# Performance work log

Hardware: AMD Instinct MI355X
Metric: run time of the kernel (lower is better)

The kernel has to match this reference:

```python
import jax, jax.numpy as jnp
import numpy as np

D, J, K, H = 4, 256, 512, 512  # d, num_output, num_input, num_hidden
B = 1024


def setup_inputs() -> dict:
    key = jax.random.key(0)
    ks = jax.random.split(key, 8)
    x = jax.random.normal(ks[0], (B, K), dtype=jnp.float32)
    # self.w = ((1-0.1)*U + 0.1) / num_input, shape [d, num_output, num_input]
    w = ((0.9 * jax.random.uniform(ks[1], (D, J, K), dtype=jnp.float32) + 0.1) / K)
    # Stacked per-output-MLP params (nn.Linear default init scale 1/sqrt(fan_in))
    s0 = 1.0 / np.sqrt(K)
    s1 = 1.0 / np.sqrt(H)
    W0 = jax.random.uniform(ks[2], (J, H, K), dtype=jnp.float32, minval=-s0, maxval=s0)
    b0 = jax.random.uniform(ks[3], (J, H), dtype=jnp.float32, minval=-s0, maxval=s0)
    W1 = jax.random.uniform(ks[4], (J, H), dtype=jnp.float32, minval=-s1, maxval=s1)  # [J,1,H] squeezed
    b1 = jax.random.uniform(ks[5], (J,), dtype=jnp.float32, minval=-s1, maxval=s1)
    logvar = jnp.ones((D,), dtype=jnp.float32) * -4.0
    return {"x": x, "i": 0, "w": w, "W0": W0, "b0": b0, "W1": W1, "b1": b1, "logvar": logvar}


def reference(x, i, w, W0, b0, W1, b1, logvar):
    # For each output j: mu[:, j] = lin1_j(LeakyReLU(lin0_j(w[i, j] * x)))
    # Fused as a single grouped GEMM over j: fold the mask w[i] into the contraction.
    wi = w[i]                                   # [J, K]
    h = jnp.einsum('jhk,jk,bk->bjh', W0, wi, x) + b0[None, :, :]   # [B, J, H]
    h = jax.nn.leaky_relu(h, negative_slope=0.01)
    mu = jnp.einsum('bjh,jh->bj', h, W1) + b1[None, :]             # [B, J]
    return (mu, logvar)
```

## Files before the change

kernel.cpp:

```cpp
#include <hip/hip_runtime.h>

#define J_ 256
#define K_ 512
#define H_ 512
#define B_ 1024
#define BK 64

typedef float f32x4 __attribute__((ext_vector_type(4)));
typedef unsigned int u32x4 __attribute__((ext_vector_type(4)));
typedef unsigned short u16x4 __attribute__((ext_vector_type(4)));
typedef unsigned short u16x8 __attribute__((ext_vector_type(8)));
typedef __bf16 bf16x8 __attribute__((ext_vector_type(8)));

__device__ __forceinline__ unsigned short f2bf(float f) {
    unsigned int u = __float_as_uint(f);
    u += 0x7fffu + ((u >> 16) & 1u);
    return (unsigned short)(u >> 16);
}

__global__ __launch_bounds__(256) void prep_kernel(
    const float* __restrict__ x, const float* __restrict__ b1,
    const float* __restrict__ logvar, unsigned short* __restrict__ xbf,
    float* __restrict__ out) {
    int t = blockIdx.x * 256 + threadIdx.x;
    {
        f32x4 v = *(const f32x4*)(x + (size_t)t * 4);
        u16x4 o;
        o[0] = f2bf(v[0]); o[1] = f2bf(v[1]); o[2] = f2bf(v[2]); o[3] = f2bf(v[3]);
        *(u16x4*)(xbf + (size_t)t * 4) = o;
    }
    if (t < (B_ * J_) / 4) {
        int b = t >> 6;
        int j4 = (t & 63) << 2;
        f32x4 bb = *(const f32x4*)(b1 + j4);
        *(f32x4*)(out + ((size_t)b << 8) + j4) = bb;
    }
    if (t < 4) out[B_ * J_ + t] = logvar[t];
}

__global__ __launch_bounds__(256, 2) void enc_kernel(
    const unsigned short* __restrict__ xbf,
    const float* __restrict__ W0,
    const float* __restrict__ wmask,
    const int* __restrict__ ip,
    const float* __restrict__ b0,
    const float* __restrict__ W1,
    float* __restrict__ out) {
    __shared__ unsigned char ldsA[128 * 128];
    __shared__ unsigned char ldsB[128 * 128];

    int p = blockIdx.x;
    int xcd = p & 7;
    int q = p >> 3;
    int j = (xcd << 5) + (q >> 5);
    int inner = q & 31;
    int m0 = (inner >> 2) << 7;
    int h0 = (inner & 3) << 7;

    int i = ip[0];
    const float* w0j = W0 + (size_t)j * (H_ * K_);
    const float* wij = wmask + ((size_t)i * J_ + j) * K_;

    int tid = threadIdx.x;
    int lane = tid & 63;
    int wv = tid >> 6;
    int wm = wv >> 1, wn = wv & 1;
    int lr = lane & 15, lg = lane >> 4;

    int srow0 = tid >> 3;
    int c = tid & 7;

    f32x4 acc[4][4] = {};

    for (int ks = 0; ks < K_ / BK; ++ks) {
        int k0 = ks * BK;
        #pragma unroll
        for (int it = 0; it < 4; ++it) {
            int r = srow0 + it * 32;
            u32x4 v = *(const u32x4*)(xbf + (size_t)(m0 + r) * K_ + k0 + c * 8);
            *(u32x4*)(ldsA + r * 128 + ((c * 16) ^ ((r & 7) << 4))) = v;
        }
        f32x4 s0 = *(const f32x4*)(wij + k0 + c * 8);
        f32x4 s1 = *(const f32x4*)(wij + k0 + c * 8 + 4);
        #pragma unroll
        for (int it = 0; it < 4; ++it) {
            int hr = srow0 + it * 32;
            const float* src = w0j + (size_t)(h0 + hr) * K_ + k0 + c * 8;
            f32x4 a0 = *(const f32x4*)(src);
            f32x4 a1 = *(const f32x4*)(src + 4);
            a0 *= s0; a1 *= s1;
            u16x8 bv;
            #pragma unroll
            for (int e = 0; e < 4; ++e) { bv[e] = f2bf(a0[e]); bv[e + 4] = f2bf(a1[e]); }
            *(u16x8*)(ldsB + hr * 128 + ((c * 16) ^ ((hr & 7) << 4))) = bv;
        }
        __syncthreads();
        #pragma unroll
        for (int kf = 0; kf < 2; ++kf) {
            bf16x8 af[4], bfr[4];
            #pragma unroll
            for (int mf = 0; mf < 4; ++mf) {
                int r = (wm << 6) + (mf << 4) + lr;
                af[mf] = *(const bf16x8*)(ldsA + r * 128 +
                          (((kf << 6) + (lg << 4)) ^ ((r & 7) << 4)));
            }
            #pragma unroll
            for (int nf = 0; nf < 4; ++nf) {
                int hrw = (wn << 6) + (nf << 4) + lr;
                bfr[nf] = *(const bf16x8*)(ldsB + hrw * 128 +
                          (((kf << 6) + (lg << 4)) ^ ((hrw & 7) << 4)));
            }
            #pragma unroll
            for (int mf = 0; mf < 4; ++mf)
                #pragma unroll
                for (int nf = 0; nf < 4; ++nf)
                    acc[mf][nf] = __builtin_amdgcn_mfma_f32_16x16x32_bf16(
                        af[mf], bfr[nf], acc[mf][nf], 0, 0, 0);
        }
        __syncthreads();
    }

    float b0v[4], w1v[4];
    #pragma unroll
    for (int nf = 0; nf < 4; ++nf) {
        int h = h0 + (wn << 6) + (nf << 4) + lr;
        b0v[nf] = b0[(size_t)j * H_ + h];
        w1v[nf] = W1[(size_t)j * H_ + h];
    }
    #pragma unroll
    for (int mf = 0; mf < 4; ++mf) {
        #pragma unroll
        for (int rg = 0; rg < 4; ++rg) {
            float ps = 0.f;
            #pragma unroll
            for (int nf = 0; nf < 4; ++nf) {
                float hv = acc[mf][nf][rg] + b0v[nf];
                hv = hv > 0.f ? hv : 0.01f * hv;
                ps += hv * w1v[nf];
            }
            ps += __shfl_xor(ps, 1);
            ps += __shfl_xor(ps, 2);
            ps += __shfl_xor(ps, 4);
            ps += __shfl_xor(ps, 8);
            if (lr == 0) {
                int row = m0 + (wm << 6) + (mf << 4) + (lg << 2) + rg;
                atomicAdd(out + (size_t)row * J_ + j, ps);
            }
        }
    }
}

extern "C" void kernel_launch(void* const* d_in, const int* in_sizes, int n_in,
                              void* d_out, int out_size, void* d_ws, size_t ws_size,
                              hipStream_t stream) {
    const float* x      = (const float*)d_in[0];
    const int*   ip     = (const int*)d_in[1];
    const float* wmask  = (const float*)d_in[2];
    const float* W0     = (const float*)d_in[3];
    const float* b0     = (const float*)d_in[4];
    const float* W1     = (const float*)d_in[5];
    const float* b1     = (const float*)d_in[6];
    const float* logvar = (const float*)d_in[7];
    float* out = (float*)d_out;
    unsigned short* xbf = (unsigned short*)d_ws;

    prep_kernel<<<512, 256, 0, stream>>>(x, b1, logvar, xbf, out);
    enc_kernel<<<8192, 256, 0, stream>>>(xbf, W0, wmask, ip, b0, W1, out);
}
```

Measured before the change: 582.9 us.

## Pre-convert masked W0 to bf16 and stream tiles via global_load_lds

Measured after the change: 582.4 us. About the same (-0.1%).

```diff
diff --git a/kernel.cpp b/kernel.cpp
--- a/kernel.cpp
+++ b/kernel.cpp
@@ -16,6 +16,12 @@
     unsigned int u = __float_as_uint(f);
     u += 0x7fffu + ((u >> 16) & 1u);
     return (unsigned short)(u >> 16);
+}
+
+__device__ __forceinline__ void gload_lds16(const void* g, void* l) {
+    __builtin_amdgcn_global_load_lds(
+        (const __attribute__((address_space(1))) unsigned int*)g,
+        (__attribute__((address_space(3))) unsigned int*)l, 16, 0, 0);
 }
 
 __global__ __launch_bounds__(256) void prep_kernel(
@@ -38,7 +44,122 @@
     if (t < 4) out[B_ * J_ + t] = logvar[t];
 }
 
-__global__ __launch_bounds__(256, 2) void enc_kernel(
+__global__ __launch_bounds__(256) void wprep_kernel(
+    const float* __restrict__ W0, const float* __restrict__ wmask,
+    const int* __restrict__ ip, unsigned short* __restrict__ w0p) {
+    size_t t = (size_t)blockIdx.x * 256 + threadIdx.x;
+    size_t e = t * 8;
+    int j = (int)(e >> 18);
+    int k = (int)(e & (K_ - 1));
+    const float* wi = wmask + ((size_t)ip[0] * J_ + j) * K_ + k;
+    f32x4 s0 = *(const f32x4*)wi;
+    f32x4 s1 = *(const f32x4*)(wi + 4);
+    f32x4 a0 = *(const f32x4*)(W0 + e);
+    f32x4 a1 = *(const f32x4*)(W0 + e + 4);
+    a0 *= s0; a1 *= s1;
+    u16x8 o;
+    #pragma unroll
+    for (int q = 0; q < 4; ++q) { o[q] = f2bf(a0[q]); o[q + 4] = f2bf(a1[q]); }
+    *(u16x8*)(w0p + e) = o;
+}
+
+__global__ __launch_bounds__(256, 3) void enc_kernel(
+    const unsigned short* __restrict__ xbf,
+    const unsigned short* __restrict__ w0p,
+    const float* __restrict__ b0,
+    const float* __restrict__ W1,
+    float* __restrict__ out) {
+    __shared__ unsigned char ldsA[128 * 128];
+    __shared__ unsigned char ldsB[128 * 128];
+
+    int p = blockIdx.x;
+    int xcd = p & 7;
+    int q = p >> 3;
+    int j = (xcd << 5) + (q >> 5);
+    int inner = q & 31;
+    int m0 = (inner >> 2) << 7;
+    int h0 = (inner & 3) << 7;
+
+    int tid = threadIdx.x;
+    int lane = tid & 63;
+    int wv = tid >> 6;
+    int wm = wv >> 1, wn = wv & 1;
+    int lr = lane & 15, lg = lane >> 4;
+    int lrow = lane >> 3;
+    int lch = lane & 7;
+    int sch = ((lch ^ lrow) << 3);
+
+    const unsigned short* aBase = xbf + (size_t)(m0 + wv * 32 + lrow) * K_ + sch;
+    const unsigned short* bBase = w0p + ((size_t)j * H_ + h0 + wv * 32 + lrow) * K_ + sch;
+    unsigned char* laBase = ldsA + wv * 4096;
+    unsigned char* lbBase = ldsB + wv * 4096;
+
+    f32x4 acc[4][4] = {};
+
+    for (int ks = 0; ks < K_ / BK; ++ks) {
+        int k0 = ks * BK;
+        #pragma unroll
+        for (int ii = 0; ii < 4; ++ii) {
+            gload_lds16(aBase + (size_t)ii * 8 * K_ + k0, laBase + ii * 1024);
+            gload_lds16(bBase + (size_t)ii * 8 * K_ + k0, lbBase + ii * 1024);
+        }
+        __syncthreads();
+        #pragma unroll
+        for (int kf = 0; kf < 2; ++kf) {
+            bf16x8 af[4], bfr[4];
+            #pragma unroll
+            for (int mf = 0; mf < 4; ++mf) {
+                int r = (wm << 6) + (mf << 4) + lr;
+                af[mf] = *(const bf16x8*)(ldsA + r * 128 +
+                          (((kf << 6) + (lg << 4)) ^ ((r & 7) << 4)));
+            }
+            #pragma unroll
+            for (int nf = 0; nf < 4; ++nf) {
+                int hrw = (wn << 6) + (nf << 4) + lr;
+                bfr[nf] = *(const bf16x8*)(ldsB + hrw * 128 +
+                          (((kf << 6) + (lg << 4)) ^ ((hrw & 7) << 4)));
+            }
+            #pragma unroll
+            for (int mf = 0; mf < 4; ++mf)
+                #pragma unroll
+                for (int nf = 0; nf < 4; ++nf)
+                    acc[mf][nf] = __builtin_amdgcn_mfma_f32_16x16x32_bf16(
+                        af[mf], bfr[nf], acc[mf][nf], 0, 0, 0);
+        }
+        __syncthreads();
+    }
+
+    float b0v[4], w1v[4];
+    #pragma unroll
+    for (int nf = 0; nf < 4; ++nf) {
+        int h = h0 + (wn << 6) + (nf << 4) + lr;
+        b0v[nf] = b0[(size_t)j * H_ + h];
+        w1v[nf] = W1[(size_t)j * H_ + h];
+    }
+    #pragma unroll
+    for (int mf = 0; mf < 4; ++mf) {
+        #pragma unroll
+        for (int rg = 0; rg < 4; ++rg) {
+            float ps = 0.f;
+            #pragma unroll
+            for (int nf = 0; nf < 4; ++nf) {
+                float hv = acc[mf][nf][rg] + b0v[nf];
+                hv = hv > 0.f ? hv : 0.01f * hv;
+                ps += hv * w1v[nf];
+            }
+            ps += __shfl_xor(ps, 1);
+            ps += __shfl_xor(ps, 2);
+            ps += __shfl_xor(ps, 4);
+            ps += __shfl_xor(ps, 8);
+            if (lr == 0) {
+                int row = m0 + (wm << 6) + (mf << 4) + (lg << 2) + rg;
+                atomicAdd(out + (size_t)row * J_ + j, ps);
+            }
+        }
+    }
+}
+
+__global__ __launch_bounds__(256, 2) void enc_kernel_fb(
     const unsigned short* __restrict__ xbf,
     const float* __restrict__ W0,
     const float* __restrict__ wmask,
@@ -66,7 +187,6 @@
     int wv = tid >> 6;
     int wm = wv >> 1, wn = wv & 1;
     int lr = lane & 15, lg = lane >> 4;
-
     int srow0 = tid >> 3;
     int c = tid & 7;
 
@@ -163,7 +283,16 @@
     const float* logvar = (const float*)d_in[7];
     float* out = (float*)d_out;
     unsigned short* xbf = (unsigned short*)d_ws;
+    const size_t xbf_elems = (size_t)B_ * K_;
+    const size_t w0p_bytes = (size_t)J_ * H_ * K_ * 2;
+    const size_t need = xbf_elems * 2 + w0p_bytes;
 
     prep_kernel<<<512, 256, 0, stream>>>(x, b1, logvar, xbf, out);
-    enc_kernel<<<8192, 256, 0, stream>>>(xbf, W0, wmask, ip, b0, W1, out);
-}
+    if (ws_size >= need) {
+        unsigned short* w0p = xbf + xbf_elems;
+        wprep_kernel<<<32768, 256, 0, stream>>>(W0, wmask, ip, w0p);
+        enc_kernel<<<8192, 256, 0, stream>>>(xbf, w0p, b0, W1, out);
+    } else {
+        enc_kernel_fb<<<8192, 256, 0, stream>>>(xbf, W0, wmask, ip, b0, W1, out);
+    }
+}
```

## Keep masked W0 slice resident in LDS and loop over all batch tiles

Applied to the files above, without the earlier changes.

Result: no change. 573.1 us (-1.7%).

```diff
diff --git a/kernel.cpp b/kernel.cpp
--- a/kernel.cpp
+++ b/kernel.cpp
@@ -7,7 +7,6 @@
 #define BK 64
 
 typedef float f32x4 __attribute__((ext_vector_type(4)));
-typedef unsigned int u32x4 __attribute__((ext_vector_type(4)));
 typedef unsigned short u16x4 __attribute__((ext_vector_type(4)));
 typedef unsigned short u16x8 __attribute__((ext_vector_type(8)));
 typedef __bf16 bf16x8 __attribute__((ext_vector_type(8)));
@@ -16,6 +15,12 @@
     unsigned int u = __float_as_uint(f);
     u += 0x7fffu + ((u >> 16) & 1u);
     return (unsigned short)(u >> 16);
+}
+
+__device__ __forceinline__ void gload_lds16(const void* g, void* l) {
+    __builtin_amdgcn_global_load_lds(
+        (const __attribute__((address_space(1))) unsigned int*)g,
+        (__attribute__((address_space(3))) unsigned int*)l, 16, 0, 0);
 }
 
 __global__ __launch_bounds__(256) void prep_kernel(
@@ -46,105 +51,111 @@
     const float* __restrict__ b0,
     const float* __restrict__ W1,
     float* __restrict__ out) {
-    __shared__ unsigned char ldsA[128 * 128];
-    __shared__ unsigned char ldsB[128 * 128];
+    __shared__ unsigned char ldsB[64 * 1024];
+    __shared__ unsigned char ldsX[128 * 128];
 
     int p = blockIdx.x;
-    int xcd = p & 7;
-    int q = p >> 3;
-    int j = (xcd << 5) + (q >> 5);
-    int inner = q & 31;
-    int m0 = (inner >> 2) << 7;
-    int h0 = (inner & 3) << 7;
-
-    int i = ip[0];
-    const float* w0j = W0 + (size_t)j * (H_ * K_);
-    const float* wij = wmask + ((size_t)i * J_ + j) * K_;
+    int j = p >> 3;
+    int hb = p & 7;
+    int h0 = hb << 6;
 
     int tid = threadIdx.x;
     int lane = tid & 63;
     int wv = tid >> 6;
-    int wm = wv >> 1, wn = wv & 1;
     int lr = lane & 15, lg = lane >> 4;
 
-    int srow0 = tid >> 3;
-    int c = tid & 7;
+    {
+        const float* w0p = W0 + ((size_t)j * H_ + h0) * K_;
+        const float* wij = wmask + ((size_t)ip[0] * J_ + j) * K_;
+        int row = (wv << 4) + lr;
+        int cb = lg;
+        const float* src = w0p + (size_t)row * K_;
+        unsigned int swb = ((unsigned)row & 7u) << 4;
+        unsigned char* dst = ldsB + row * 1024;
+        #pragma unroll
+        for (int qq = 0; qq < 16; ++qq) {
+            int c = cb + (qq << 2);
+            int k = c << 3;
+            f32x4 a0 = *(const f32x4*)(src + k);
+            f32x4 a1 = *(const f32x4*)(src + k + 4);
+            f32x4 s0 = *(const f32x4*)(wij + k);
+            f32x4 s1 = *(const f32x4*)(wij + k + 4);
+            a0 *= s0; a1 *= s1;
+            u16x8 o;
+            #pragma unroll
+            for (int e = 0; e < 4; ++e) { o[e] = f2bf(a0[e]); o[e + 4] = f2bf(a1[e]); }
+            *(u16x8*)(dst + (((unsigned)c << 4) ^ swb)) = o;
+        }
+    }
 
-    f32x4 acc[4][4] = {};
-
-    for (int ks = 0; ks < K_ / BK; ++ks) {
-        int k0 = ks * BK;
-        #pragma unroll
-        for (int it = 0; it < 4; ++it) {
-            int r = srow0 + it * 32;
-            u32x4 v = *(const u32x4*)(xbf + (size_t)(m0 + r) * K_ + k0 + c * 8);
-            *(u32x4*)(ldsA + r * 128 + ((c * 16) ^ ((r & 7) << 4))) = v;
-        }
-        f32x4 s0 = *(const f32x4*)(wij + k0 + c * 8);
-        f32x4 s1 = *(const f32x4*)(wij + k0 + c * 8 + 4);
-        #pragma unroll
-        for (int it = 0; it < 4; ++it) {
-            int hr = srow0 + it * 32;
-            const float* src = w0j + (size_t)(h0 + hr) * K_ + k0 + c * 8;
-            f32x4 a0 = *(const f32x4*)(src);
-            f32x4 a1 = *(const f32x4*)(src + 4);
-            a0 *= s0; a1 *= s1;
-            u16x8 bv;
-            #pragma unroll
-            for (int e = 0; e < 4; ++e) { bv[e] = f2bf(a0[e]); bv[e + 4] = f2bf(a1[e]); }
-            *(u16x8*)(ldsB + hr * 128 + ((c * 16) ^ ((hr & 7) << 4))) = bv;
-        }
-        __syncthreads();
-        #pragma unroll
-        for (int kf = 0; kf < 2; ++kf) {
-            bf16x8 af[4], bfr[4];
-            #pragma unroll
-            for (int mf = 0; mf < 4; ++mf) {
-                int r = (wm << 6) + (mf << 4) + lr;
-                af[mf] = *(const bf16x8*)(ldsA + r * 128 +
-                          (((kf << 6) + (lg << 4)) ^ ((r & 7) << 4)));
-            }
-            #pragma unroll
-            for (int nf = 0; nf < 4; ++nf) {
-                int hrw = (wn << 6) + (nf << 4) + lr;
-                bfr[nf] = *(const bf16x8*)(ldsB + hrw * 128 +
-                          (((kf << 6) + (lg << 4)) ^ ((hrw & 7) << 4)));
-            }
-            #pragma unroll
-            for (int mf = 0; mf < 4; ++mf)
-                #pragma unroll
-                for (int nf = 0; nf < 4; ++nf)
-                    acc[mf][nf] = __builtin_amdgcn_mfma_f32_16x16x32_bf16(
-                        af[mf], bfr[nf], acc[mf][nf], 0, 0, 0);
-        }
-        __syncthreads();
-    }
+    int lrow = lane >> 3;
+    int lch = lane & 7;
+    int sch = ((lch ^ lrow) << 3);
+    const unsigned short* aBase = xbf + (size_t)(wv * 32 + lrow) * K_ + sch;
+    unsigned char* laBase = ldsX + wv * 4096;
 
     float b0v[4], w1v[4];
     #pragma unroll
     for (int nf = 0; nf < 4; ++nf) {
-        int h = h0 + (wn << 6) + (nf << 4) + lr;
-        b0v[nf] = b0[(size_t)j * H_ + h];
-        w1v[nf] = W1[(size_t)j * H_ + h];
+        int col = h0 + (nf << 4) + lr;
+        b0v[nf] = b0[(size_t)j * H_ + col];
+        w1v[nf] = W1[(size_t)j * H_ + col];
     }
-    #pragma unroll
-    for (int mf = 0; mf < 4; ++mf) {
+
+    __syncthreads();
+
+    for (int mt = 0; mt < 8; ++mt) {
+        int m0 = mt << 7;
+        f32x4 acc[2][4] = {};
+        for (int ks = 0; ks < 8; ++ks) {
+            int k0 = ks * BK;
+            #pragma unroll
+            for (int ii = 0; ii < 4; ++ii)
+                gload_lds16(aBase + (size_t)(m0 + ii * 8) * K_ + k0, laBase + ii * 1024);
+            __syncthreads();
+            #pragma unroll
+            for (int kf = 0; kf < 2; ++kf) {
+                bf16x8 af[2], bfv[4];
+                #pragma unroll
+                for (int mf = 0; mf < 2; ++mf) {
+                    int r = (wv << 5) + (mf << 4) + lr;
+                    af[mf] = *(const bf16x8*)(ldsX + r * 128 +
+                              (((kf << 6) + (lg << 4)) ^ ((r & 7) << 4)));
+                }
+                #pragma unroll
+                for (int nf = 0; nf < 4; ++nf) {
+                    int row = (nf << 4) + lr;
+                    bfv[nf] = *(const bf16x8*)(ldsB + row * 1024 +
+                              (((ks << 7) + (kf << 6) + (lg << 4)) ^ ((row & 7) << 4)));
+                }
+                #pragma unroll
+                for (int mf = 0; mf < 2; ++mf)
+                    #pragma unroll
+                    for (int nf = 0; nf < 4; ++nf)
+                        acc[mf][nf] = __builtin_amdgcn_mfma_f32_16x16x32_bf16(
+                            af[mf], bfv[nf], acc[mf][nf], 0, 0, 0);
+            }
+            __syncthreads();
+        }
         #pragma unroll
-        for (int rg = 0; rg < 4; ++rg) {
-            float ps = 0.f;
+        for (int mf = 0; mf < 2; ++mf) {
             #pragma unroll
-            for (int nf = 0; nf < 4; ++nf) {
-                float hv = acc[mf][nf][rg] + b0v[nf];
-                hv = hv > 0.f ? hv : 0.01f * hv;
-                ps += hv * w1v[nf];
-            }
-            ps += __shfl_xor(ps, 1);
-            ps += __shfl_xor(ps, 2);
-            ps += __shfl_xor(ps, 4);
-            ps += __shfl_xor(ps, 8);
-            if (lr == 0) {
-                int row = m0 + (wm << 6) + (mf << 4) + (lg << 2) + rg;
-                atomicAdd(out + (size_t)row * J_ + j, ps);
+            for (int rg = 0; rg < 4; ++rg) {
+                float ps = 0.f;
+                #pragma unroll
+                for (int nf = 0; nf < 4; ++nf) {
+                    float hv = acc[mf][nf][rg] + b0v[nf];
+                    hv = hv > 0.f ? hv : 0.01f * hv;
+                    ps += hv * w1v[nf];
+                }
+                ps += __shfl_xor(ps, 1);
+                ps += __shfl_xor(ps, 2);
+                ps += __shfl_xor(ps, 4);
+                ps += __shfl_xor(ps, 8);
+                if (lr == 0) {
+                    int row = m0 + (wv << 5) + (mf << 4) + (lg << 2) + rg;
+                    atomicAdd(out + (size_t)row * J_ + j, ps);
+                }
             }
         }
     }
@@ -165,5 +176,5 @@
     unsigned short* xbf = (unsigned short*)d_ws;
 
     prep_kernel<<<512, 256, 0, stream>>>(x, b1, logvar, xbf, out);
-    enc_kernel<<<8192, 256, 0, stream>>>(xbf, W0, wmask, ip, b0, W1, out);
+    enc_kernel<<<2048, 256, 0, stream>>>(xbf, W0, wmask, ip, b0, W1, out);
 }
```
